# Kernel tuning notes

Measured on AMD Instinct MI355X. Metric: run time of the kernel, lower is better.

The kernel has to match this reference:

```python
import jax, jax.numpy as jnp
import numpy as np
import math

F, M, C, OUT = 60, 600, 8, 18  # feature_size, max_samples, cluster_size, output_dim
B = 2048


def l2_normalize(x, axis):
    # matches tf.nn.l2_normalize (epsilon=1e-12)
    sq = jnp.sum(jnp.square(x), axis=axis, keepdims=True)
    return x * jax.lax.rsqrt(jnp.maximum(sq, 1e-12))


def setup_inputs() -> dict:
    key = jax.random.key(0)
    k = jax.random.split(key, 6)
    s1 = 1.0 / math.sqrt(F)
    s2 = 1.0 / math.sqrt(C)
    return {
        "reshaped_input": jax.random.normal(k[0], (B * M, F), dtype=jnp.float32),
        "cluster_weights": jax.random.normal(k[1], (F, C), dtype=jnp.float32) * s1,
        "covar_weights": jax.random.normal(k[2], (F, C), dtype=jnp.float32) * s1,
        "cluster_biases": jax.random.normal(k[3], (C,), dtype=jnp.float32) * s1,
        "cluster_weights2": jax.random.normal(k[4], (1, F, C), dtype=jnp.float32) * s1,
        "hidden1_weights": jax.random.normal(k[5], (2 * C * F, OUT), dtype=jnp.float32) * s2,
    }


def reference(reshaped_input, cluster_weights, covar_weights, cluster_biases,
              cluster_weights2, hidden1_weights):
    cw = jnp.square(covar_weights) + 1e-6                      # [F, C]

    act = reshaped_input @ cluster_weights + cluster_biases    # [B*M, C]
    act = jax.nn.softmax(act, axis=-1)
    act = act.reshape(-1, M, C)                                # [B, M, C]

    a_sum = jnp.sum(act, axis=-2, keepdims=True)               # [B, 1, C]
    a = a_sum * cluster_weights2                               # [B, F, C]

    x = reshaped_input.reshape(-1, M, F)                       # [B, M, F]

    fv1 = jnp.einsum('bmc,bmf->bfc', act, x)                   # [B, F, C]
    fv2 = jnp.einsum('bmc,bmf->bfc', act, jnp.square(x))       # [B, F, C]

    a2 = a_sum * jnp.square(cluster_weights2)                  # [B, F, C]
    b2 = fv1 * cluster_weights2                                # [B, F, C]

    fv2 = a2 + fv2 - 2.0 * b2
    fv2 = fv2 / jnp.square(cw)
    fv2 = fv2 - a_sum                                          # broadcast [B,1,C]
    fv2 = fv2.reshape(-1, C * F)
    fv2 = l2_normalize(fv2, axis=1)
    fv2 = l2_normalize(fv2, axis=1)  # second normalize as in original (idempotent)

    fv1 = (fv1 - a) / cw                                       # [B, F, C]
    fv1 = l2_normalize(fv1, axis=1)                            # per-cluster, along F
    fv1 = fv1.reshape(-1, C * F)
    fv1 = l2_normalize(fv1, axis=1)

    fv = jnp.concatenate([fv1, fv2], axis=1)                   # [B, 2*C*F]
    return fv @ hidden1_weights                                # [B, OUT]
```

## Files before the change

kernel.cpp:

```cpp
#include <hip/hip_runtime.h>
#include <hip/hip_bf16.h>

#define FDIM 60
#define MROW 600
#define CDIM 8
#define ODIM 18
#define CH   128
#define NCHUNK 5
#define BLK  512

typedef short bf16x8 __attribute__((ext_vector_type(8)));
typedef float f32x4  __attribute__((ext_vector_type(4)));

__device__ __forceinline__ unsigned int pk2(float lo, float hi) {
    __hip_bfloat162 h2 = __float22bfloat162_rn(make_float2(lo, hi));
    unsigned int u;
    __builtin_memcpy(&u, &h2, sizeof(u));
    return u;
}
__device__ __forceinline__ short f2bf(float f) {
    __hip_bfloat16 h = __float2bfloat16(f);
    short s;
    __builtin_memcpy(&s, &h, sizeof(s));
    return s;
}

__global__ void __launch_bounds__(BLK, 6) netfv_kernel(
    const float* __restrict__ x,
    const float* __restrict__ W,
    const float* __restrict__ covar,
    const float* __restrict__ bias,
    const float* __restrict__ cw2,
    const float* __restrict__ H,
    float* __restrict__ out)
{
    __shared__ __align__(16) short xsT1[64 * 136];
    __shared__ __align__(16) short xsT2[64 * 136];
    __shared__ __align__(16) short actT[16 * 136];
    __shared__ __align__(16) short WtB [16 * 72];
    __shared__ __align__(16) float fvbuf[1024];
    __shared__ __align__(16) float fvl[960];
    __shared__ float redA[64], redB[64];
    __shared__ float asuml[8], n1rs[8], n1c_s[8], n2c_s[8], scal[2];

    const int tid  = threadIdx.x;
    const int b    = blockIdx.x;
    const int lane = tid & 63;
    const int wv   = tid >> 6;
    const int mg   = tid >> 3;
    const int fs   = tid & 7;
    const int ln15 = lane & 15;
    const int quad = lane >> 4;
    const int fvsel = wv & 1;
    const int tile  = wv >> 1;

    const size_t rowbase = (size_t)b * (MROW * FDIM);
    const float* prow = x + rowbase + (size_t)(2 * mg) * FDIM + 8 * fs;

    float4 A0, A1, B0, B1;
    B0 = B1 = make_float4(0.f, 0.f, 0.f, 0.f);
    A0 = *(const float4*)prow;
    A1 = *(const float4*)(prow + FDIM);
    if (fs < 7) { B0 = *(const float4*)(prow + 4); B1 = *(const float4*)(prow + FDIM + 4); }

    {
        int c = tid >> 5, j = tid & 31;
        float v0 = (2 * j     < FDIM) ? W[(2 * j) * CDIM + (c & 7)]     : 0.f;
        float v1 = (2 * j + 1 < FDIM) ? W[(2 * j + 1) * CDIM + (c & 7)] : 0.f;
        if (c >= CDIM) { v0 = 0.f; v1 = 0.f; }
        ((unsigned int*)WtB)[c * 36 + j] = pk2(v0, v1);
    }
    {
        unsigned int* az = (unsigned int*)(actT + 8 * 136);
        for (int i = tid; i < 544; i += BLK) az[i] = 0u;
    }
    __syncthreads();

    const bf16x8 aw0 = *(const bf16x8*)(WtB + ln15 * 72 + quad * 8);
    const bf16x8 aw1 = *(const bf16x8*)(WtB + ln15 * 72 + 32 + quad * 8);
    const float4 lb  = *(const float4*)(bias + (quad & 1) * 4);

    f32x4 acc = {0.f, 0.f, 0.f, 0.f};
    float asum_acc[4] = {0.f, 0.f, 0.f, 0.f};
    const int mloc = wv * 16 + ln15;

    for (int ck = 0; ck < NCHUNK; ++ck) {
        const bool valid = (ck * CH + 2 * mg) < MROW;

        float4 nA0, nA1, nB0, nB1;
        nA0 = nA1 = nB0 = nB1 = make_float4(0.f, 0.f, 0.f, 0.f);
        if (ck + 1 < NCHUNK && ((ck + 1) * CH + 2 * mg) < MROW) {
            const float* pn = prow + (size_t)(ck + 1) * (CH * FDIM);
            nA0 = *(const float4*)pn;
            nA1 = *(const float4*)(pn + FDIM);
            if (fs < 7) { nB0 = *(const float4*)(pn + 4); nB1 = *(const float4*)(pn + FDIM + 4); }
        }

        const int grow = ck * CH + mloc;
        const bool vm = grow < MROW;
        const float* xr = x + rowbase + (size_t)(vm ? grow : (MROW - 1)) * FDIM;
        float4 c0 = *(const float4*)(xr + quad * 8);
        float4 c1 = *(const float4*)(xr + quad * 8 + 4);
        float4 c2 = *(const float4*)(xr + 32 + quad * 8);
        float4 c3 = (quad < 3) ? *(const float4*)(xr + 36 + quad * 8)
                               : make_float4(0.f, 0.f, 0.f, 0.f);

        if (valid) {
            float xv0[8] = {A0.x, A0.y, A0.z, A0.w, B0.x, B0.y, B0.z, B0.w};
            float xv1[8] = {A1.x, A1.y, A1.z, A1.w, B1.x, B1.y, B1.z, B1.w};
            const int wbase = (((mg >> 2) ^ fs) << 2) + (mg & 3);
            #pragma unroll
            for (int i = 0; i < 8; ++i) {
                int woff = (8 * fs + i) * 68 + wbase;
                ((unsigned int*)xsT1)[woff] = pk2(xv0[i], xv1[i]);
                ((unsigned int*)xsT2)[woff] = pk2(xv0[i] * xv0[i], xv1[i] * xv1[i]);
            }
        }

        {
            union { bf16x8 v; unsigned int u[4]; } Lo, Hi;
            Lo.u[0] = pk2(c0.x, c0.y); Lo.u[1] = pk2(c0.z, c0.w);
            Lo.u[2] = pk2(c1.x, c1.y); Lo.u[3] = pk2(c1.z, c1.w);
            Hi.u[0] = pk2(c2.x, c2.y); Hi.u[1] = pk2(c2.z, c2.w);
            Hi.u[2] = pk2(c3.x, c3.y); Hi.u[3] = pk2(c3.z, c3.w);
            f32x4 lz = {0.f, 0.f, 0.f, 0.f};
            lz = __builtin_amdgcn_mfma_f32_16x16x32_bf16(aw0, Lo.v, lz, 0, 0, 0);
            lz = __builtin_amdgcn_mfma_f32_16x16x32_bf16(aw1, Hi.v, lz, 0, 0, 0);
            float L0 = lz[0] + lb.x, L1 = lz[1] + lb.y;
            float L2 = lz[2] + lb.z, L3 = lz[3] + lb.w;
            float mx = fmaxf(fmaxf(L0, L1), fmaxf(L2, L3));
            mx = fmaxf(mx, __shfl_xor(mx, 16));
            float e0 = __expf(L0 - mx), e1 = __expf(L1 - mx);
            float e2 = __expf(L2 - mx), e3 = __expf(L3 - mx);
            float s = e0 + e1 + e2 + e3;
            s += __shfl_xor(s, 16);
            float inv = __builtin_amdgcn_rcpf(s);
            if (quad < 2) {
                float a0  = vm ? e0 * inv : 0.f, a1v = vm ? e1 * inv : 0.f;
                float a2v = vm ? e2 * inv : 0.f, a3v = vm ? e3 * inv : 0.f;
                asum_acc[0] += a0;  asum_acc[1] += a1v;
                asum_acc[2] += a2v; asum_acc[3] += a3v;
                actT[(quad * 4 + 0) * 136 + mloc] = f2bf(a0);
                actT[(quad * 4 + 1) * 136 + mloc] = f2bf(a1v);
                actT[(quad * 4 + 2) * 136 + mloc] = f2bf(a2v);
                actT[(quad * 4 + 3) * 136 + mloc] = f2bf(a3v);
            }
        }
        __syncthreads();

        {
            const short* xsel = fvsel ? xsT2 : xsT1;
            const int f   = tile * 16 + ln15;
            const int fsw = f >> 3;
            #pragma unroll
            for (int ks = 0; ks < 4; ++ks) {
                bf16x8 av = *(const bf16x8*)(actT + ln15 * 136 + ks * 32 + quad * 8);
                int kblk = ks * 4 + quad;
                bf16x8 bv = *(const bf16x8*)(xsel + f * 136 + ((kblk ^ fsw) << 3));
                acc = __builtin_amdgcn_mfma_f32_16x16x32_bf16(av, bv, acc, 0, 0, 0);
            }
        }
        __syncthreads();
        A0 = nA0; A1 = nA1; B0 = nB0; B1 = nB1;
    }

    #pragma unroll
    for (int r = 0; r < 4; ++r) {
        float v = asum_acc[r];
        v += __shfl_xor(v, 1); v += __shfl_xor(v, 2);
        v += __shfl_xor(v, 4); v += __shfl_xor(v, 8);
        asum_acc[r] = v;
    }
    if (quad < 2 && ln15 == 0) {
        #pragma unroll
        for (int r = 0; r < 4; ++r) redA[wv * 8 + quad * 4 + r] = asum_acc[r];
    }
    __syncthreads();
    if (tid < 64) {
        float v = redA[tid];
        v += __shfl_down(v, 8); v += __shfl_down(v, 16); v += __shfl_down(v, 32);
        if (tid < 8) asuml[tid] = v;
    }
    if (quad < 2) {
        #pragma unroll
        for (int r = 0; r < 4; ++r)
            fvbuf[fvsel * 512 + (tile * 16 + ln15) * 8 + quad * 4 + r] = acc[r];
    }
    __syncthreads();

    float fv1v = 0.f, fv2v = 0.f;
    const int f_e = tid >> 3, c_e = tid & 7;
    if (tid < 480) {
        float fv1r = fvbuf[f_e * 8 + c_e];
        float fv2r = fvbuf[512 + f_e * 8 + c_e];
        float asv  = asuml[c_e];
        float cw2v = cw2[f_e * 8 + c_e];
        float cv   = covar[f_e * 8 + c_e];
        float cwv  = cv * cv + 1e-6f;
        float rcw  = 1.0f / cwv;
        fv1v = (fv1r - asv * cw2v) * rcw;
        fv2v = (fmaf(asv * cw2v, cw2v, fv2r) - 2.0f * fv1r * cw2v) * rcw * rcw - asv;
    }

    {
        float p1 = fv1v * fv1v, p2 = fv2v * fv2v;
        p1 += __shfl_down(p1, 8);  p2 += __shfl_down(p2, 8);
        p1 += __shfl_down(p1, 16); p2 += __shfl_down(p2, 16);
        p1 += __shfl_down(p1, 32); p2 += __shfl_down(p2, 32);
        if (lane < 8) { redA[wv * 8 + lane] = p1; redB[wv * 8 + lane] = p2; }
    }
    __syncthreads();
    if (tid < 64) {
        float q1 = redA[tid], q2 = redB[tid];
        q1 += __shfl_down(q1, 8);  q2 += __shfl_down(q2, 8);
        q1 += __shfl_down(q1, 16); q2 += __shfl_down(q2, 16);
        q1 += __shfl_down(q1, 32); q2 += __shfl_down(q2, 32);
        if (tid < 8) { n1c_s[tid] = q1; n2c_s[tid] = q2; }
    }
    __syncthreads();
    if (tid == 0) {
        float S1 = 0.f, S2 = 0.f;
        #pragma unroll
        for (int c = 0; c < 8; ++c) {
            float rs = rsqrtf(fmaxf(n1c_s[c], 1e-12f));
            n1rs[c] = rs;
            S1 += n1c_s[c] * rs * rs;
            S2 += n2c_s[c];
        }
        scal[0] = rsqrtf(fmaxf(S1, 1e-12f));
        scal[1] = rsqrtf(fmaxf(S2, 1e-12f));
    }
    __syncthreads();
    if (tid < 480) {
        fvl[f_e * 8 + c_e]       = fv1v * n1rs[c_e] * scal[0];
        fvl[480 + f_e * 8 + c_e] = fv2v * scal[1];
    }
    __syncthreads();

    for (int o = wv; o < ODIM; o += 8) {
        float sacc = 0.f;
        #pragma unroll 5
        for (int i = lane; i < 960; i += 64)
            sacc = fmaf(fvl[i], H[i * ODIM + o], sacc);
        sacc += __shfl_down(sacc, 32);
        sacc += __shfl_down(sacc, 16);
        sacc += __shfl_down(sacc, 8);
        sacc += __shfl_down(sacc, 4);
        sacc += __shfl_down(sacc, 2);
        sacc += __shfl_down(sacc, 1);
        if (lane == 0) out[(size_t)b * ODIM + o] = sacc;
    }
}

extern "C" void kernel_launch(void* const* d_in, const int* in_sizes, int n_in,
                              void* d_out, int out_size, void* d_ws, size_t ws_size,
                              hipStream_t stream) {
    const float* x     = (const float*)d_in[0];
    const float* W     = (const float*)d_in[1];
    const float* covar = (const float*)d_in[2];
    const float* bias  = (const float*)d_in[3];
    const float* cw2   = (const float*)d_in[4];
    const float* H     = (const float*)d_in[5];
    float* outp = (float*)d_out;

    const int Bn = in_sizes[0] / (MROW * FDIM);
    hipLaunchKernelGGL(netfv_kernel, dim3(Bn), dim3(BLK), 0, stream,
                       x, W, covar, bias, cw2, H, outp);
}
```

Before: 482.8 us.

## Stage input rows in LDS to avoid a second global read for logits

Each chunk's input rows are now packed to bf16 row-major in a new shared buffer, xsM. The logit MFMA reads its operands from there instead of issuing a second set of global float4 loads for the same rows. Chunk size changes to 120 so five chunks cover the 600 rows exactly, which removes the per-chunk tail validity checks; the transposed buffers are zero-initialized instead. Block barriers become raw s_barrier with explicit lgkm waits, and only a wave-local wait is used before the logit read. The cost is about 22KB more LDS per block and a lower launch-bounds occupancy hint, which may reduce the number of resident blocks.

```diff
diff --git a/kernel.cpp b/kernel.cpp
--- a/kernel.cpp
+++ b/kernel.cpp
@@ -5,7 +5,7 @@
 #define MROW 600
 #define CDIM 8
 #define ODIM 18
-#define CH   128
+#define CH   120
 #define NCHUNK 5
 #define BLK  512
 
@@ -25,7 +25,17 @@
     return s;
 }
 
-__global__ void __launch_bounds__(BLK, 6) netfv_kernel(
+#define WAVE_LGKM() do {                                          \
+    asm volatile("s_waitcnt lgkmcnt(0)" ::: "memory");            \
+    __builtin_amdgcn_sched_barrier(0);                            \
+} while (0)
+#define RAW_BAR() do {                                            \
+    asm volatile("s_waitcnt lgkmcnt(0)" ::: "memory");            \
+    __builtin_amdgcn_s_barrier();                                 \
+    __builtin_amdgcn_sched_barrier(0);                            \
+} while (0)
+
+__global__ void __launch_bounds__(BLK, 4) netfv_kernel(
     const float* __restrict__ x,
     const float* __restrict__ W,
     const float* __restrict__ covar,
@@ -36,6 +46,7 @@
 {
     __shared__ __align__(16) short xsT1[64 * 136];
     __shared__ __align__(16) short xsT2[64 * 136];
+    __shared__ __align__(16) short xsM [128 * 88];
     __shared__ __align__(16) short actT[16 * 136];
     __shared__ __align__(16) short WtB [16 * 72];
     __shared__ __align__(16) float fvbuf[1024];
@@ -55,13 +66,18 @@
     const int tile  = wv >> 1;
 
     const size_t rowbase = (size_t)b * (MROW * FDIM);
+    const bool stv = (mg < 60);
     const float* prow = x + rowbase + (size_t)(2 * mg) * FDIM + 8 * fs;
+    const int mloc = wv * 16 + ln15;
+    const bool vm = (mloc < CH);
 
     float4 A0, A1, B0, B1;
-    B0 = B1 = make_float4(0.f, 0.f, 0.f, 0.f);
-    A0 = *(const float4*)prow;
-    A1 = *(const float4*)(prow + FDIM);
-    if (fs < 7) { B0 = *(const float4*)(prow + 4); B1 = *(const float4*)(prow + FDIM + 4); }
+    A0 = A1 = B0 = B1 = make_float4(0.f, 0.f, 0.f, 0.f);
+    if (stv) {
+        A0 = *(const float4*)prow;
+        A1 = *(const float4*)(prow + FDIM);
+        if (fs < 7) { B0 = *(const float4*)(prow + 4); B1 = *(const float4*)(prow + FDIM + 4); }
+    }
 
     {
         int c = tid >> 5, j = tid & 31;
@@ -71,6 +87,11 @@
         ((unsigned int*)WtB)[c * 36 + j] = pk2(v0, v1);
     }
     {
+        unsigned int* z1 = (unsigned int*)xsT1;
+        unsigned int* z2 = (unsigned int*)xsT2;
+        for (int i = tid; i < 64 * 68; i += BLK) { z1[i] = 0u; z2[i] = 0u; }
+        unsigned int* zm = (unsigned int*)(xsM + 120 * 88);
+        for (int i = tid; i < 8 * 44; i += BLK) zm[i] = 0u;
         unsigned int* az = (unsigned int*)(actT + 8 * 136);
         for (int i = tid; i < 544; i += BLK) az[i] = 0u;
     }
@@ -82,32 +103,28 @@
 
     f32x4 acc = {0.f, 0.f, 0.f, 0.f};
     float asum_acc[4] = {0.f, 0.f, 0.f, 0.f};
-    const int mloc = wv * 16 + ln15;
 
     for (int ck = 0; ck < NCHUNK; ++ck) {
-        const bool valid = (ck * CH + 2 * mg) < MROW;
-
         float4 nA0, nA1, nB0, nB1;
         nA0 = nA1 = nB0 = nB1 = make_float4(0.f, 0.f, 0.f, 0.f);
-        if (ck + 1 < NCHUNK && ((ck + 1) * CH + 2 * mg) < MROW) {
+        if (ck + 1 < NCHUNK && stv) {
             const float* pn = prow + (size_t)(ck + 1) * (CH * FDIM);
             nA0 = *(const float4*)pn;
             nA1 = *(const float4*)(pn + FDIM);
             if (fs < 7) { nB0 = *(const float4*)(pn + 4); nB1 = *(const float4*)(pn + FDIM + 4); }
         }
 
-        const int grow = ck * CH + mloc;
-        const bool vm = grow < MROW;
-        const float* xr = x + rowbase + (size_t)(vm ? grow : (MROW - 1)) * FDIM;
-        float4 c0 = *(const float4*)(xr + quad * 8);
-        float4 c1 = *(const float4*)(xr + quad * 8 + 4);
-        float4 c2 = *(const float4*)(xr + 32 + quad * 8);
-        float4 c3 = (quad < 3) ? *(const float4*)(xr + 36 + quad * 8)
-                               : make_float4(0.f, 0.f, 0.f, 0.f);
-
-        if (valid) {
+        if (stv) {
             float xv0[8] = {A0.x, A0.y, A0.z, A0.w, B0.x, B0.y, B0.z, B0.w};
             float xv1[8] = {A1.x, A1.y, A1.z, A1.w, B1.x, B1.y, B1.z, B1.w};
+            {
+                unsigned int q0 = pk2(xv0[0], xv0[1]), q1 = pk2(xv0[2], xv0[3]);
+                unsigned int q2 = pk2(xv0[4], xv0[5]), q3 = pk2(xv0[6], xv0[7]);
+                *(uint4*)(xsM + (2 * mg) * 88 + 8 * fs) = make_uint4(q0, q1, q2, q3);
+                unsigned int s0 = pk2(xv1[0], xv1[1]), s1 = pk2(xv1[2], xv1[3]);
+                unsigned int s2 = pk2(xv1[4], xv1[5]), s3 = pk2(xv1[6], xv1[7]);
+                *(uint4*)(xsM + (2 * mg + 1) * 88 + 8 * fs) = make_uint4(s0, s1, s2, s3);
+            }
             const int wbase = (((mg >> 2) ^ fs) << 2) + (mg & 3);
             #pragma unroll
             for (int i = 0; i < 8; ++i) {
@@ -117,15 +134,13 @@
             }
         }
 
+        WAVE_LGKM();
         {
-            union { bf16x8 v; unsigned int u[4]; } Lo, Hi;
-            Lo.u[0] = pk2(c0.x, c0.y); Lo.u[1] = pk2(c0.z, c0.w);
-            Lo.u[2] = pk2(c1.x, c1.y); Lo.u[3] = pk2(c1.z, c1.w);
-            Hi.u[0] = pk2(c2.x, c2.y); Hi.u[1] = pk2(c2.z, c2.w);
-            Hi.u[2] = pk2(c3.x, c3.y); Hi.u[3] = pk2(c3.z, c3.w);
+            bf16x8 bv0 = *(const bf16x8*)(xsM + mloc * 88 + quad * 8);
+            bf16x8 bv1 = *(const bf16x8*)(xsM + mloc * 88 + 32 + quad * 8);
             f32x4 lz = {0.f, 0.f, 0.f, 0.f};
-            lz = __builtin_amdgcn_mfma_f32_16x16x32_bf16(aw0, Lo.v, lz, 0, 0, 0);
-            lz = __builtin_amdgcn_mfma_f32_16x16x32_bf16(aw1, Hi.v, lz, 0, 0, 0);
+            lz = __builtin_amdgcn_mfma_f32_16x16x32_bf16(aw0, bv0, lz, 0, 0, 0);
+            lz = __builtin_amdgcn_mfma_f32_16x16x32_bf16(aw1, bv1, lz, 0, 0, 0);
             float L0 = lz[0] + lb.x, L1 = lz[1] + lb.y;
             float L2 = lz[2] + lb.z, L3 = lz[3] + lb.w;
             float mx = fmaxf(fmaxf(L0, L1), fmaxf(L2, L3));
@@ -146,7 +161,7 @@
                 actT[(quad * 4 + 3) * 136 + mloc] = f2bf(a3v);
             }
         }
-        __syncthreads();
+        RAW_BAR();
 
         {
             const short* xsel = fvsel ? xsT2 : xsT1;
@@ -160,7 +175,8 @@
                 acc = __builtin_amdgcn_mfma_f32_16x16x32_bf16(av, bv, acc, 0, 0, 0);
             }
         }
-        __syncthreads();
+        RAW_BAR();
+
         A0 = nA0; A1 = nA1; B0 = nB0; B1 = nB1;
     }
 
```

Result: faster. 432.3 us (-10.5%).
